# Kernel tuning notes

Hardware: AMD Instinct MI355X
Metric: run time of the kernel (lower is better)

The kernel has to match this reference:

```python
import jax, jax.numpy as jnp
import numpy as np

T, N, D = 512, 32, 1024
H, P, L = 1024, 1024, 4
STDV = 1.0 / np.sqrt(H)


def setup_inputs() -> dict:
    key = jax.random.key(0)
    ks = jax.random.split(key, 11)
    u = lambda k, shape: jax.random.uniform(k, shape, jnp.float32, -STDV, STDV)
    return {
        "x": jax.random.normal(ks[0], (T, N, D), jnp.float32),
        "h0": jax.random.normal(ks[1], (L, N, P), jnp.float32),
        "c0": jax.random.normal(ks[2], (L, N, H), jnp.float32),
        "w_ih": u(ks[3], (L, D, 4 * H)),
        "w_hh": u(ks[4], (L, P, 4 * H)),
        "b_ih": u(ks[5], (L, 4 * H)),
        "b_hh": u(ks[6], (L, 4 * H)),
        "w_ic": u(ks[7], (L, H)),
        "w_fc": u(ks[8], (L, H)),
        "w_oc": u(ks[9], (L, H)),
        "w_hm": u(ks[10], (L, H, P)),
    }


def _run_layer(x, h0, c0, wih, whh, b, wic, wfc, woc, whm):
    # x: (T, N, Din); h0: (N, P); c0: (N, H)
    def step(carry, xt):
        h, c = carry
        a = xt @ wih + h @ whh + b  # (N, 4H)
        ai, af, ag, ao = jnp.split(a, 4, axis=1)
        i = jax.nn.sigmoid(ai + c * wic)
        f = jax.nn.sigmoid(af + c * wfc)
        g = jnp.tanh(ag)
        nc = f * c + i * g
        o = jax.nn.sigmoid(ao + nc * woc)
        nh = (o * jnp.tanh(nc)) @ whm  # projection -> (N, P)
        return (nh, nc), nh

    (hT, cT), ys = jax.lax.scan(step, (h0, c0), x)
    return ys, hT, cT


def reference(x, h0, c0, w_ih, w_hh, b_ih, b_hh, w_ic, w_fc, w_oc, w_hm):
    layer_input = x
    hs, cs = [], []
    for l in range(L):
        b = b_ih[l] + b_hh[l]
        layer_input, hT, cT = _run_layer(
            layer_input, h0[l], c0[l], w_ih[l], w_hh[l], b,
            w_ic[l], w_fc[l], w_oc[l], w_hm[l])
        hs.append(hT)
        cs.append(cT)
    return layer_input, jnp.stack(hs, 0), jnp.stack(cs, 0)
```

## Files before the change

kernel.cpp:

```cpp
#include <hip/hip_runtime.h>
#include <hip/hip_bf16.h>
#include <cstdint>
#include <cstddef>


#define TT 512
#define NBATCH 32
#define HID 1024
#define G4 4096
#define KCAT 2048

typedef __attribute__((ext_vector_type(4))) float f32x4;
typedef __attribute__((ext_vector_type(8))) short bf16x8;

static __device__ __forceinline__ uint16_t f2bf(float f) {
  uint32_t u = __builtin_bit_cast(uint32_t, f);
  uint32_t lsb = (u >> 16) & 1u;
  u += 0x7fffu + lsb;
  return (uint16_t)(u >> 16);
}

static __device__ __forceinline__ f32x4 mfma16x16(bf16x8 a, bf16x8 b, f32x4 c) {
  return __builtin_amdgcn_mfma_f32_16x16x32_bf16(a, b, c, 0, 0, 0);
}

static __device__ __forceinline__ float sigm(float v) { return 1.f / (1.f + __expf(-v)); }
static __device__ __forceinline__ float tanh_(float v) {
  float a = fabsf(v);
  float e = __expf(-2.f * a);
  float t = (1.f - e) / (1.f + e);
  return v < 0.f ? -t : t;
}

__global__ void __launch_bounds__(256) add_bias(const float* __restrict__ a,
                                                const float* __restrict__ b,
                                                float* __restrict__ o, int n) {
  int i = blockIdx.x * 256 + threadIdx.x;
  if (i < n) o[i] = a[i] + b[i];
}

__global__ void __launch_bounds__(256) cast_bf16(const float* __restrict__ src,
                                                 uint16_t* __restrict__ dst, int n8) {
  int i = blockIdx.x * 256 + threadIdx.x;
  if (i >= n8) return;
  const float* s = src + (size_t)i * 8;
  f32x4 v0 = *(const f32x4*)s;
  f32x4 v1 = *(const f32x4*)(s + 4);
  bf16x8 o;
  o[0] = (short)f2bf(v0[0]); o[1] = (short)f2bf(v0[1]);
  o[2] = (short)f2bf(v0[2]); o[3] = (short)f2bf(v0[3]);
  o[4] = (short)f2bf(v1[0]); o[5] = (short)f2bf(v1[1]);
  o[6] = (short)f2bf(v1[2]); o[7] = (short)f2bf(v1[3]);
  *(bf16x8*)(dst + (size_t)i * 8) = o;
}

__global__ void __launch_bounds__(256) transpose_cast(const float* __restrict__ src, int lds,
                                                      uint16_t* __restrict__ dst, int ldd) {
  const int k0 = blockIdx.x * 64;
  const int n0 = blockIdx.y * 64;
  __shared__ float tile[64][65];
  const int tid = threadIdx.x;
#pragma unroll
  for (int p = 0; p < 4; ++p) {
    int kk = (tid >> 4) + 16 * p, nq = tid & 15;
    f32x4 v = *(const f32x4*)(src + (size_t)(k0 + kk) * lds + n0 + 4 * nq);
#pragma unroll
    for (int j = 0; j < 4; ++j) tile[kk][4 * nq + j] = v[j];
  }
  __syncthreads();
#pragma unroll
  for (int p = 0; p < 2; ++p) {
    int nn = (tid >> 3) + 32 * p, kq = tid & 7;
    bf16x8 o;
#pragma unroll
    for (int i = 0; i < 8; ++i) o[i] = (short)f2bf(tile[8 * kq + i][nn]);
    *(bf16x8*)(dst + (size_t)(n0 + nn) * ldd + k0 + 8 * kq) = o;
  }
}

template <bool OBF16>
__global__ void __launch_bounds__(256) gemm_tn(const uint16_t* __restrict__ A, int lda, int M,
                                               const uint16_t* __restrict__ Bt, int ldb,
                                               void* __restrict__ Cp, int ldc, int K) {
  const int m0 = blockIdx.x * 128, n0 = blockIdx.y * 128;
  __shared__ __align__(16) uint16_t As[128 * 40];
  __shared__ __align__(16) uint16_t Bs[128 * 40];
  const int tid = threadIdx.x;
  const int w = tid >> 6, lane = tid & 63, r16 = lane & 15, g = lane >> 4;
  f32x4 acc[4][4];
#pragma unroll
  for (int a = 0; a < 4; ++a)
#pragma unroll
    for (int b = 0; b < 4; ++b) acc[a][b] = (f32x4){0.f, 0.f, 0.f, 0.f};

  for (int k0 = 0; k0 < K; k0 += 32) {
#pragma unroll
    for (int q = 0; q < 2; ++q) {
      int c = q * 256 + tid, row = c >> 2, col = (c & 3) * 8;
      bf16x8 va = (bf16x8){0, 0, 0, 0, 0, 0, 0, 0};
      if (m0 + row < M) va = *(const bf16x8*)(A + (size_t)(m0 + row) * lda + k0 + col);
      *(bf16x8*)(As + row * 40 + col) = va;
      bf16x8 vb = *(const bf16x8*)(Bt + (size_t)(n0 + row) * ldb + k0 + col);
      *(bf16x8*)(Bs + row * 40 + col) = vb;
    }
    __syncthreads();
    bf16x8 bfr[4];
#pragma unroll
    for (int nf = 0; nf < 4; ++nf)
      bfr[nf] = *(const bf16x8*)(Bs + ((w >> 1) * 64 + nf * 16 + r16) * 40 + 8 * g);
#pragma unroll
    for (int mf = 0; mf < 4; ++mf) {
      bf16x8 a = *(const bf16x8*)(As + ((w & 1) * 64 + mf * 16 + r16) * 40 + 8 * g);
#pragma unroll
      for (int nf = 0; nf < 4; ++nf) acc[mf][nf] = mfma16x16(a, bfr[nf], acc[mf][nf]);
    }
    __syncthreads();
  }
#pragma unroll
  for (int mf = 0; mf < 4; ++mf)
#pragma unroll
    for (int nf = 0; nf < 4; ++nf)
#pragma unroll
      for (int reg = 0; reg < 4; ++reg) {
        int row = m0 + (w & 1) * 64 + mf * 16 + (lane >> 4) * 4 + reg;
        int col = n0 + (w >> 1) * 64 + nf * 16 + (lane & 15);
        if (row < M) {
          if (OBF16)
            ((uint16_t*)Cp)[(size_t)row * ldc + col] = f2bf(acc[mf][nf][reg]);
          else
            ((float*)Cp)[(size_t)row * ldc + col] = acc[mf][nf][reg];
        }
      }
}

__global__ void __launch_bounds__(256) gemm32_f32(const float* __restrict__ A, int lda,
                                                  const float* __restrict__ B, int ldb,
                                                  float* __restrict__ C, int ldc, int K) {
  const int n0 = blockIdx.x * 64;
  __shared__ __align__(16) uint16_t As[32 * 40];
  __shared__ __align__(16) uint16_t Bs[64 * 40];
  const int tid = threadIdx.x;
  const int w = tid >> 6, lane = tid & 63, r16 = lane & 15, g = lane >> 4;
  f32x4 acc[2];
  acc[0] = (f32x4){0.f, 0.f, 0.f, 0.f};
  acc[1] = acc[0];
  for (int k0 = 0; k0 < K; k0 += 32) {
    {
      int m = tid >> 3, kq = tid & 7;
      f32x4 v = *(const f32x4*)(A + (size_t)m * lda + k0 + 4 * kq);
      uint64_t pk = (uint64_t)f2bf(v[0]) | ((uint64_t)f2bf(v[1]) << 16) |
                    ((uint64_t)f2bf(v[2]) << 32) | ((uint64_t)f2bf(v[3]) << 48);
      *(uint64_t*)(As + m * 40 + 4 * kq) = pk;
    }
#pragma unroll
    for (int p = 0; p < 2; ++p) {
      int k = (tid >> 4) + 16 * p, nq = tid & 15;
      f32x4 v = *(const f32x4*)(B + (size_t)(k0 + k) * ldb + n0 + 4 * nq);
#pragma unroll
      for (int j = 0; j < 4; ++j) Bs[(4 * nq + j) * 40 + k] = f2bf(v[j]);
    }
    __syncthreads();
    bf16x8 a0 = *(const bf16x8*)(As + r16 * 40 + 8 * g);
    bf16x8 a1 = *(const bf16x8*)(As + (r16 + 16) * 40 + 8 * g);
    bf16x8 b = *(const bf16x8*)(Bs + (16 * w + r16) * 40 + 8 * g);
    acc[0] = mfma16x16(a0, b, acc[0]);
    acc[1] = mfma16x16(a1, b, acc[1]);
    __syncthreads();
  }
#pragma unroll
  for (int rt = 0; rt < 2; ++rt)
#pragma unroll
    for (int reg = 0; reg < 4; ++reg)
      C[(size_t)(16 * rt + 4 * g + reg) * ldc + n0 + 16 * w + r16] = acc[rt][reg];
}

__global__ void __launch_bounds__(512) lstm_slot(int slot, const uint16_t* __restrict__ xbf,
                                                 const float* __restrict__ wic,
                                                 const float* __restrict__ wfc,
                                                 const float* __restrict__ woc,
                                                 const float* __restrict__ r0,
                                                 const float* __restrict__ bias,
                                                 float* __restrict__ cstate,
                                                 const uint16_t* __restrict__ Wcat,
                                                 uint16_t* __restrict__ ring,
                                                 uint16_t* __restrict__ m3) {
  const int blk = blockIdx.x;
  const int l = blk >> 6;
  const int slc = blk & 63;
  const int t = slot - l;
  if (t < 0 || t >= TT) return;

  __shared__ __align__(16) float red[16384];
  const int tid = threadIdx.x;
  const int w = tid >> 6, lane = tid & 63;
  const int r16 = lane & 15, g = lane >> 4;
  const int j0 = slc * 16;
  const uint16_t* Wl = Wcat + (size_t)l * G4 * KCAT;

  f32x4 acc[2][4];
#pragma unroll
  for (int a = 0; a < 2; ++a)
#pragma unroll
    for (int b = 0; b < 4; ++b) acc[a][b] = (f32x4){0.f, 0.f, 0.f, 0.f};

  {
    const uint16_t* s0 = (l == 0) ? xbf + (size_t)t * (NBATCH * HID)
                                  : ring + ((size_t)(l - 1) * 2 + (t & 1)) * (NBATCH * HID);
#pragma unroll
    for (int i = 0; i < 4; ++i) {
      const int k0 = (i * 8 + w) * 32;
      bf16x8 a0 = *(const bf16x8*)(s0 + r16 * HID + k0 + 8 * g);
      bf16x8 a1 = *(const bf16x8*)(s0 + (r16 + 16) * HID + k0 + 8 * g);
#pragma unroll
      for (int s = 0; s < 4; ++s) {
        bf16x8 b = *(const bf16x8*)(Wl + (size_t)(s * 1024 + j0 + r16) * KCAT + k0 + 8 * g);
        acc[0][s] = mfma16x16(a0, b, acc[0][s]);
        acc[1][s] = mfma16x16(a1, b, acc[1][s]);
      }
    }
  }
  if (t > 0) {
    const uint16_t* s1 = (l < 3) ? ring + ((size_t)l * 2 + ((t - 1) & 1)) * (NBATCH * HID)
                                 : m3 + (size_t)(t - 1) * (NBATCH * HID);
#pragma unroll
    for (int i = 0; i < 4; ++i) {
      const int k0 = (i * 8 + w) * 32;
      bf16x8 a0 = *(const bf16x8*)(s1 + r16 * HID + k0 + 8 * g);
      bf16x8 a1 = *(const bf16x8*)(s1 + (r16 + 16) * HID + k0 + 8 * g);
#pragma unroll
      for (int s = 0; s < 4; ++s) {
        bf16x8 b =
            *(const bf16x8*)(Wl + (size_t)(s * 1024 + j0 + r16) * KCAT + 1024 + k0 + 8 * g);
        acc[0][s] = mfma16x16(a0, b, acc[0][s]);
        acc[1][s] = mfma16x16(a1, b, acc[1][s]);
      }
    }
  }

#pragma unroll
  for (int rt = 0; rt < 2; ++rt)
#pragma unroll
    for (int s = 0; s < 4; ++s)
      *(f32x4*)(red + (size_t)((w * 8 + rt * 4 + s) * 64 + lane) * 4) = acc[rt][s];
  __syncthreads();

  {
    const int r = tid >> 4, jj = tid & 15;
    const int rt = r >> 4, reg = r & 3;
    const int lanec = ((r & 15) >> 2) * 16 + jj;
    float gate[4];
#pragma unroll
    for (int s = 0; s < 4; ++s) {
      float v = 0.f;
#pragma unroll
      for (int w2 = 0; w2 < 8; ++w2)
        v += red[(size_t)((w2 * 8 + rt * 4 + s) * 64 + lanec) * 4 + reg];
      gate[s] = v;
    }
    const int hj = j0 + jj;
    const float* bl = bias + l * G4;
    float ai = gate[0] + bl[hj];
    float af = gate[1] + bl[1024 + hj];
    float ag = gate[2] + bl[2048 + hj];
    float ao = gate[3] + bl[3072 + hj];
    if (t == 0) {
      const float* r0l = r0 + ((size_t)l * NBATCH + r) * G4;
      ai += r0l[hj];
      af += r0l[1024 + hj];
      ag += r0l[2048 + hj];
      ao += r0l[3072 + hj];
    }
    float* cl = cstate + ((size_t)l * NBATCH + r) * HID;
    float cold = cl[hj];
    float iv = sigm(ai + cold * wic[l * HID + hj]);
    float fv = sigm(af + cold * wfc[l * HID + hj]);
    float gv = tanh_(ag);
    float nc = fv * cold + iv * gv;
    float ov = sigm(ao + nc * woc[l * HID + hj]);
    float mv = ov * tanh_(nc);
    cl[hj] = nc;
    uint16_t* mout = ((l < 3) ? ring + ((size_t)l * 2 + (t & 1)) * (NBATCH * HID)
                              : m3 + (size_t)t * (NBATCH * HID)) +
                     (size_t)r * HID;
    mout[hj] = f2bf(mv);
  }
}

extern "C" void kernel_launch(void* const* d_in, const int* in_sizes, int n_in, void* d_out,
                              int out_size, void* d_ws, size_t ws_size, hipStream_t stream) {
  (void)in_sizes; (void)n_in; (void)out_size; (void)ws_size;
  const float* x = (const float*)d_in[0];
  const float* h0 = (const float*)d_in[1];
  const float* c0 = (const float*)d_in[2];
  const float* wih = (const float*)d_in[3];
  const float* whh = (const float*)d_in[4];
  const float* bih = (const float*)d_in[5];
  const float* bhh = (const float*)d_in[6];
  const float* wic = (const float*)d_in[7];
  const float* wfc = (const float*)d_in[8];
  const float* woc = (const float*)d_in[9];
  const float* whm = (const float*)d_in[10];

  float* ys = (float*)d_out;
  float* hs = ys + (size_t)TT * NBATCH * HID;
  float* cs = hs + (size_t)4 * NBATCH * HID;

  uint8_t* ws = (uint8_t*)d_ws;
  uint16_t* Wcat = (uint16_t*)(ws);
  uint16_t* m3 = (uint16_t*)(ws + 67108864ull);
  uint16_t* wihT = m3;
  uint16_t* xbf = (uint16_t*)(ws + 100663296ull);
  uint16_t* whhT = xbf;
  uint16_t* whm_bf = (uint16_t*)(ws + 134217728ull);
  uint16_t* whmT = (uint16_t*)(ws + 142606336ull);
  uint16_t* ring = (uint16_t*)(ws + 150994944ull);
  float* r0 = (float*)(ws + 151388160ull);
  float* bias = (float*)(ws + 153485312ull);

  hipMemcpyAsync(cs, c0, (size_t)4 * NBATCH * HID * sizeof(float), hipMemcpyDeviceToDevice,
                 stream);
  add_bias<<<64, 256, 0, stream>>>(bih, bhh, bias, 4 * G4);
  cast_bf16<<<2048, 256, 0, stream>>>(whm, whm_bf, 524288);
  for (int l = 0; l < 4; ++l)
    transpose_cast<<<dim3(16, 16), 256, 0, stream>>>(whm + (size_t)l * 1048576, 1024,
                                                     whmT + (size_t)l * 1048576, 1024);
  transpose_cast<<<dim3(16, 64), 256, 0, stream>>>(wih, G4, Wcat, KCAT);
  for (int l = 1; l < 4; ++l)
    transpose_cast<<<dim3(16, 64), 256, 0, stream>>>(wih + (size_t)l * 4194304, G4,
                                                     wihT + (size_t)(l - 1) * 4194304, 1024);
  for (int l = 0; l < 4; ++l)
    transpose_cast<<<dim3(16, 64), 256, 0, stream>>>(whh + (size_t)l * 4194304, G4,
                                                     whhT + (size_t)l * 4194304, 1024);
  for (int l = 1; l < 4; ++l)
    gemm_tn<true><<<dim3(32, 8), 256, 0, stream>>>(
        wihT + (size_t)(l - 1) * 4194304, 1024, 4096, whm_bf + (size_t)(l - 1) * 1048576, 1024,
        Wcat + (size_t)l * 8388608, KCAT, 1024);
  for (int l = 0; l < 4; ++l)
    gemm_tn<true><<<dim3(32, 8), 256, 0, stream>>>(
        whhT + (size_t)l * 4194304, 1024, 4096, whm_bf + (size_t)l * 1048576, 1024,
        Wcat + (size_t)l * 8388608 + 1024, KCAT, 1024);
  for (int l = 0; l < 4; ++l)
    gemm32_f32<<<64, 256, 0, stream>>>(h0 + (size_t)l * 32768, 1024,
                                       whh + (size_t)l * 4194304, G4, r0 + (size_t)l * 131072,
                                       G4, 1024);
  cast_bf16<<<8192, 256, 0, stream>>>(x, xbf, 2097152);

  for (int s = 0; s < TT + 3; ++s)
    lstm_slot<<<256, 512, 0, stream>>>(s, xbf, wic, wfc, woc, r0, bias, cs, Wcat, ring, m3);

  gemm_tn<false><<<dim3(128, 8), 256, 0, stream>>>(m3, 1024, 16384,
                                                   whmT + (size_t)3 * 1048576, 1024, ys, 1024,
                                                   1024);
  for (int l = 0; l < 4; ++l) {
    const uint16_t* mlast = (l < 3) ? ring + ((size_t)l * 2 + 1) * (NBATCH * HID)
                                    : m3 + (size_t)(TT - 1) * (NBATCH * HID);
    gemm_tn<false><<<dim3(1, 8), 256, 0, stream>>>(mlast, 1024, 32,
                                                   whmT + (size_t)l * 1048576, 1024,
                                                   hs + (size_t)l * 32768, 1024, 1024);
  }
}
```

Before: 8.593 ms.

## Replace per-timestep launches with a persistent cooperative kernel and grid barrier

The 515 per-slot launches of the wavefront LSTM kernel become one cooperative persistent kernel that loops over slots and synchronises with a hierarchical atomic grid barrier. Each block keeps its slice of the fused weight matrix in registers across all steps instead of reloading it from global memory, and keeps the cell state, bias and peephole weights in registers. This removes launch overhead and repeated weight traffic, at the cost of heavy register pressure (bf16x8 breg[2][4][4] with launch_bounds 512,2) and reliance on all 256 blocks being co-resident.

```diff
diff --git a/kernel.cpp b/kernel.cpp
--- a/kernel.cpp
+++ b/kernel.cpp
@@ -174,116 +174,157 @@
       C[(size_t)(16 * rt + 4 * g + reg) * ldc + n0 + 16 * w + r16] = acc[rt][reg];
 }
 
-__global__ void __launch_bounds__(512) lstm_slot(int slot, const uint16_t* __restrict__ xbf,
-                                                 const float* __restrict__ wic,
-                                                 const float* __restrict__ wfc,
-                                                 const float* __restrict__ woc,
-                                                 const float* __restrict__ r0,
-                                                 const float* __restrict__ bias,
-                                                 float* __restrict__ cstate,
-                                                 const uint16_t* __restrict__ Wcat,
-                                                 uint16_t* __restrict__ ring,
-                                                 uint16_t* __restrict__ m3) {
+static __device__ __forceinline__ void grid_barrier(uint32_t* sync) {
+  __syncthreads();
+  if (threadIdx.x == 0) {
+    uint32_t* grp = sync + 16 * (blockIdx.x >> 5);
+    uint32_t* root = sync + 128;
+    uint32_t* gen = sync + 144;
+    uint32_t g = __hip_atomic_load(gen, __ATOMIC_RELAXED, __HIP_MEMORY_SCOPE_AGENT);
+    uint32_t v = __hip_atomic_fetch_add(grp, 1u, __ATOMIC_ACQ_REL, __HIP_MEMORY_SCOPE_AGENT);
+    bool bumped = false;
+    if (v == 31u) {
+      __hip_atomic_store(grp, 0u, __ATOMIC_RELAXED, __HIP_MEMORY_SCOPE_AGENT);
+      uint32_t r = __hip_atomic_fetch_add(root, 1u, __ATOMIC_ACQ_REL, __HIP_MEMORY_SCOPE_AGENT);
+      if (r == 7u) {
+        __hip_atomic_store(root, 0u, __ATOMIC_RELAXED, __HIP_MEMORY_SCOPE_AGENT);
+        __hip_atomic_fetch_add(gen, 1u, __ATOMIC_RELEASE, __HIP_MEMORY_SCOPE_AGENT);
+        bumped = true;
+      }
+    }
+    if (!bumped) {
+      uint32_t cur;
+      do {
+        __builtin_amdgcn_s_sleep(2);
+        cur = __hip_atomic_load(gen, __ATOMIC_RELAXED, __HIP_MEMORY_SCOPE_AGENT);
+      } while (cur == g);
+      (void)__hip_atomic_load(gen, __ATOMIC_ACQUIRE, __HIP_MEMORY_SCOPE_AGENT);
+    }
+  }
+  __syncthreads();
+}
+
+__global__ void __launch_bounds__(512, 2) lstm_persist(
+    const uint16_t* __restrict__ xbf, const float* __restrict__ wic,
+    const float* __restrict__ wfc, const float* __restrict__ woc,
+    const float* __restrict__ r0, const float* __restrict__ bias,
+    const float* __restrict__ c0, float* __restrict__ cs,
+    const uint16_t* __restrict__ Wcat, uint16_t* __restrict__ ring,
+    uint16_t* __restrict__ m3, uint32_t* __restrict__ sync) {
   const int blk = blockIdx.x;
-  const int l = blk >> 6;
-  const int slc = blk & 63;
-  const int t = slot - l;
-  if (t < 0 || t >= TT) return;
-
+  const int l = blk >> 6, slc = blk & 63;
+  const int j0 = slc * 16;
+  const int tid = threadIdx.x;
+  const int w = tid >> 6, lane = tid & 63, r16 = lane & 15, g = lane >> 4;
   __shared__ __align__(16) float red[16384];
-  const int tid = threadIdx.x;
-  const int w = tid >> 6, lane = tid & 63;
-  const int r16 = lane & 15, g = lane >> 4;
-  const int j0 = slc * 16;
+
   const uint16_t* Wl = Wcat + (size_t)l * G4 * KCAT;
-
-  f32x4 acc[2][4];
-#pragma unroll
-  for (int a = 0; a < 2; ++a)
-#pragma unroll
-    for (int b = 0; b < 4; ++b) acc[a][b] = (f32x4){0.f, 0.f, 0.f, 0.f};
-
-  {
-    const uint16_t* s0 = (l == 0) ? xbf + (size_t)t * (NBATCH * HID)
-                                  : ring + ((size_t)(l - 1) * 2 + (t & 1)) * (NBATCH * HID);
-#pragma unroll
-    for (int i = 0; i < 4; ++i) {
-      const int k0 = (i * 8 + w) * 32;
-      bf16x8 a0 = *(const bf16x8*)(s0 + r16 * HID + k0 + 8 * g);
-      bf16x8 a1 = *(const bf16x8*)(s0 + (r16 + 16) * HID + k0 + 8 * g);
+  bf16x8 breg[2][4][4];
+#pragma unroll
+  for (int ph = 0; ph < 2; ++ph)
+#pragma unroll
+    for (int i = 0; i < 4; ++i)
+#pragma unroll
+      for (int s = 0; s < 4; ++s)
+        breg[ph][i][s] = *(const bf16x8*)(Wl + (size_t)(s * 1024 + j0 + r16) * KCAT +
+                                          ph * 1024 + (i * 8 + w) * 32 + 8 * g);
+
+  const int pr = tid >> 4, pjj = tid & 15, phj = j0 + pjj;
+  const int prt = pr >> 4, preg = pr & 3;
+  const int planec = ((pr & 15) >> 2) * 16 + pjj;
+  const float bl0 = bias[l * G4 + phj];
+  const float bl1 = bias[l * G4 + 1024 + phj];
+  const float bl2 = bias[l * G4 + 2048 + phj];
+  const float bl3 = bias[l * G4 + 3072 + phj];
+  const float wicv = wic[l * HID + phj];
+  const float wfcv = wfc[l * HID + phj];
+  const float wocv = woc[l * HID + phj];
+  float creg = c0[(size_t)l * NBATCH * HID + (size_t)pr * HID + phj];
+
+#pragma unroll 1
+  for (int sl = 0; sl < TT + 3; ++sl) {
+    const int t = sl - l;
+    if (t >= 0 && t < TT) {
+      f32x4 acc[2][4];
+#pragma unroll
+      for (int a = 0; a < 2; ++a)
+#pragma unroll
+        for (int b = 0; b < 4; ++b) acc[a][b] = (f32x4){0.f, 0.f, 0.f, 0.f};
+
+      {
+        const uint16_t* s0 = (l == 0)
+                                 ? xbf + (size_t)t * (NBATCH * HID)
+                                 : ring + ((size_t)(l - 1) * 2 + (t & 1)) * (NBATCH * HID);
+#pragma unroll
+        for (int i = 0; i < 4; ++i) {
+          const int k0 = (i * 8 + w) * 32;
+          bf16x8 a0 = *(const bf16x8*)(s0 + r16 * HID + k0 + 8 * g);
+          bf16x8 a1 = *(const bf16x8*)(s0 + (r16 + 16) * HID + k0 + 8 * g);
+#pragma unroll
+          for (int s = 0; s < 4; ++s) {
+            acc[0][s] = mfma16x16(a0, breg[0][i][s], acc[0][s]);
+            acc[1][s] = mfma16x16(a1, breg[0][i][s], acc[1][s]);
+          }
+        }
+      }
+      if (t > 0) {
+        const uint16_t* s1 = (l < 3)
+                                 ? ring + ((size_t)l * 2 + ((t - 1) & 1)) * (NBATCH * HID)
+                                 : m3 + (size_t)(t - 1) * (NBATCH * HID);
+#pragma unroll
+        for (int i = 0; i < 4; ++i) {
+          const int k0 = (i * 8 + w) * 32;
+          bf16x8 a0 = *(const bf16x8*)(s1 + r16 * HID + k0 + 8 * g);
+          bf16x8 a1 = *(const bf16x8*)(s1 + (r16 + 16) * HID + k0 + 8 * g);
+#pragma unroll
+          for (int s = 0; s < 4; ++s) {
+            acc[0][s] = mfma16x16(a0, breg[1][i][s], acc[0][s]);
+            acc[1][s] = mfma16x16(a1, breg[1][i][s], acc[1][s]);
+          }
+        }
+      }
+
+#pragma unroll
+      for (int rt = 0; rt < 2; ++rt)
+#pragma unroll
+        for (int s = 0; s < 4; ++s)
+          *(f32x4*)(red + (size_t)((w * 8 + rt * 4 + s) * 64 + lane) * 4) = acc[rt][s];
+      __syncthreads();
+
+      float gate[4];
 #pragma unroll
       for (int s = 0; s < 4; ++s) {
-        bf16x8 b = *(const bf16x8*)(Wl + (size_t)(s * 1024 + j0 + r16) * KCAT + k0 + 8 * g);
-        acc[0][s] = mfma16x16(a0, b, acc[0][s]);
-        acc[1][s] = mfma16x16(a1, b, acc[1][s]);
-      }
-    }
-  }
-  if (t > 0) {
-    const uint16_t* s1 = (l < 3) ? ring + ((size_t)l * 2 + ((t - 1) & 1)) * (NBATCH * HID)
-                                 : m3 + (size_t)(t - 1) * (NBATCH * HID);
-#pragma unroll
-    for (int i = 0; i < 4; ++i) {
-      const int k0 = (i * 8 + w) * 32;
-      bf16x8 a0 = *(const bf16x8*)(s1 + r16 * HID + k0 + 8 * g);
-      bf16x8 a1 = *(const bf16x8*)(s1 + (r16 + 16) * HID + k0 + 8 * g);
-#pragma unroll
-      for (int s = 0; s < 4; ++s) {
-        bf16x8 b =
-            *(const bf16x8*)(Wl + (size_t)(s * 1024 + j0 + r16) * KCAT + 1024 + k0 + 8 * g);
-        acc[0][s] = mfma16x16(a0, b, acc[0][s]);
-        acc[1][s] = mfma16x16(a1, b, acc[1][s]);
-      }
-    }
-  }
-
-#pragma unroll
-  for (int rt = 0; rt < 2; ++rt)
-#pragma unroll
-    for (int s = 0; s < 4; ++s)
-      *(f32x4*)(red + (size_t)((w * 8 + rt * 4 + s) * 64 + lane) * 4) = acc[rt][s];
-  __syncthreads();
-
-  {
-    const int r = tid >> 4, jj = tid & 15;
-    const int rt = r >> 4, reg = r & 3;
-    const int lanec = ((r & 15) >> 2) * 16 + jj;
-    float gate[4];
-#pragma unroll
-    for (int s = 0; s < 4; ++s) {
-      float v = 0.f;
-#pragma unroll
-      for (int w2 = 0; w2 < 8; ++w2)
-        v += red[(size_t)((w2 * 8 + rt * 4 + s) * 64 + lanec) * 4 + reg];
-      gate[s] = v;
-    }
-    const int hj = j0 + jj;
-    const float* bl = bias + l * G4;
-    float ai = gate[0] + bl[hj];
-    float af = gate[1] + bl[1024 + hj];
-    float ag = gate[2] + bl[2048 + hj];
-    float ao = gate[3] + bl[3072 + hj];
-    if (t == 0) {
-      const float* r0l = r0 + ((size_t)l * NBATCH + r) * G4;
-      ai += r0l[hj];
-      af += r0l[1024 + hj];
-      ag += r0l[2048 + hj];
-      ao += r0l[3072 + hj];
-    }
-    float* cl = cstate + ((size_t)l * NBATCH + r) * HID;
-    float cold = cl[hj];
-    float iv = sigm(ai + cold * wic[l * HID + hj]);
-    float fv = sigm(af + cold * wfc[l * HID + hj]);
-    float gv = tanh_(ag);
-    float nc = fv * cold + iv * gv;
-    float ov = sigm(ao + nc * woc[l * HID + hj]);
-    float mv = ov * tanh_(nc);
-    cl[hj] = nc;
-    uint16_t* mout = ((l < 3) ? ring + ((size_t)l * 2 + (t & 1)) * (NBATCH * HID)
-                              : m3 + (size_t)t * (NBATCH * HID)) +
-                     (size_t)r * HID;
-    mout[hj] = f2bf(mv);
-  }
+        float v = 0.f;
+#pragma unroll
+        for (int w2 = 0; w2 < 8; ++w2)
+          v += red[(size_t)((w2 * 8 + prt * 4 + s) * 64 + planec) * 4 + preg];
+        gate[s] = v;
+      }
+      float ai = gate[0] + bl0, af = gate[1] + bl1, ag = gate[2] + bl2, ao = gate[3] + bl3;
+      if (t == 0) {
+        const float* r0l = r0 + ((size_t)l * NBATCH + pr) * G4;
+        ai += r0l[phj];
+        af += r0l[1024 + phj];
+        ag += r0l[2048 + phj];
+        ao += r0l[3072 + phj];
+      }
+      float iv = sigm(ai + creg * wicv);
+      float fv = sigm(af + creg * wfcv);
+      float gv = tanh_(ag);
+      float nc = fv * creg + iv * gv;
+      float ov = sigm(ao + nc * wocv);
+      float mv = ov * tanh_(nc);
+      creg = nc;
+      uint16_t* mout =
+          ((l < 3) ? ring + ((size_t)l * 2 + (t & 1)) * (NBATCH * HID)
+                   : m3 + (size_t)t * (NBATCH * HID)) +
+          (size_t)pr * HID;
+      mout[phj] = f2bf(mv);
+    }
+    grid_barrier(sync);
+  }
+
+  cs[(size_t)l * NBATCH * HID + (size_t)pr * HID + phj] = creg;
 }
 
 extern "C" void kernel_launch(void* const* d_in, const int* in_sizes, int n_in, void* d_out,
@@ -316,9 +357,9 @@
   uint16_t* ring = (uint16_t*)(ws + 150994944ull);
   float* r0 = (float*)(ws + 151388160ull);
   float* bias = (float*)(ws + 153485312ull);
-
-  hipMemcpyAsync(cs, c0, (size_t)4 * NBATCH * HID * sizeof(float), hipMemcpyDeviceToDevice,
-                 stream);
+  uint32_t* sync = (uint32_t*)(ws + 153550848ull);
+
+  hipMemsetAsync(sync, 0, 1024, stream);
   add_bias<<<64, 256, 0, stream>>>(bih, bhh, bias, 4 * G4);
   cast_bf16<<<2048, 256, 0, stream>>>(whm, whm_bf, 524288);
   for (int l = 0; l < 4; ++l)
@@ -345,8 +386,23 @@
                                        G4, 1024);
   cast_bf16<<<8192, 256, 0, stream>>>(x, xbf, 2097152);
 
-  for (int s = 0; s < TT + 3; ++s)
-    lstm_slot<<<256, 512, 0, stream>>>(s, xbf, wic, wfc, woc, r0, bias, cs, Wcat, ring, m3);
+  {
+    const uint16_t* a0 = xbf;
+    const float* a1 = wic;
+    const float* a2 = wfc;
+    const float* a3 = woc;
+    const float* a4 = r0;
+    const float* a5 = bias;
+    const float* a6 = c0;
+    float* a7 = cs;
+    const uint16_t* a8 = Wcat;
+    uint16_t* a9 = ring;
+    uint16_t* a10 = m3;
+    uint32_t* a11 = sync;
+    void* args[] = {&a0, &a1, &a2, &a3, &a4, &a5, &a6, &a7, &a8, &a9, &a10, &a11};
+    hipLaunchCooperativeKernel((const void*)lstm_persist, dim3(256), dim3(512), args, 0,
+                               stream);
+  }
 
   gemm_tn<false><<<dim3(128, 8), 256, 0, stream>>>(m3, 1024, 16384,
                                                    whmT + (size_t)3 * 1048576, 1024, ys, 1024,
```

After: 9.472 ms. +10.2%, slower.
